# Kernel optimization log

Measured on AMD Instinct MI355X. Metric: run time of the kernel, lower is better.

## Reference

```python
import jax, jax.numpy as jnp
import numpy as np

B, S, S2 = 4, 4096, 2048
D, SCAF_D, H = 1024, 768, 8
HD = D // H
BLEND = 0.5
SIG_HALF = 0.6224593312018546  # sigmoid(0.5), initial sparsity_factor
K = max(1, min(S, int(S * SIG_HALF)))  # 2549, static top-k size


def setup_inputs() -> dict:
    key = jax.random.key(0)
    ks = jax.random.split(key, 12)
    s = 0.02
    return {
        "base_hidden": jax.random.normal(ks[0], (B, S, D), jnp.float32),
        "scaffold_hidden": jax.random.normal(ks[1], (B, S2, SCAF_D), jnp.float32),
        "scaffold_proj_w": jax.random.normal(ks[2], (D, SCAF_D), jnp.float32) * s,
        "scaffold_proj_b": jnp.zeros((D,), jnp.float32),
        "topk_w": jax.random.normal(ks[3], (1, D), jnp.float32) * s,
        "topk_b": jnp.zeros((1,), jnp.float32),
        "in_proj_w": jax.random.normal(ks[4], (3 * D, D), jnp.float32) * s,
        "in_proj_b": jnp.zeros((3 * D,), jnp.float32),
        "out_proj_w": jax.random.normal(ks[5], (D, D), jnp.float32) * s,
        "out_proj_b": jnp.zeros((D,), jnp.float32),
        "gate_w": jax.random.normal(ks[6], (1, D), jnp.float32) * s,
        "gate_b": jnp.zeros((1,), jnp.float32),
        "confidence_threshold": jnp.array([0.65], jnp.float32),
    }


def reference(base_hidden, scaffold_hidden, scaffold_proj_w, scaffold_proj_b,
              topk_w, topk_b, in_proj_w, in_proj_b, out_proj_w, out_proj_b,
              gate_w, gate_b, confidence_threshold):
    # scaffold projection: [B,S2,SCAF_D] -> [B,S2,D]
    scaf = jnp.einsum('bsk,dk->bsd', scaffold_hidden, scaffold_proj_w) + scaffold_proj_b
    conf = jnp.mean(jnp.linalg.norm(scaf, axis=-1))

    # learned top-k token selection on base tokens
    scores = jnp.einsum('bsd,od->bso', base_hidden, topk_w)[..., 0] + topk_b[0]  # [B,S]
    _, idx = jax.lax.top_k(scores, K)  # [B,K]
    sparse = jnp.take_along_axis(base_hidden, idx[:, :, None], axis=1)  # [B,K,D]

    # multihead cross-attention: query=sparse tokens, key/value=scaffold
    wq, wk, wv = in_proj_w[:D], in_proj_w[D:2 * D], in_proj_w[2 * D:]
    bq, bk, bv = in_proj_b[:D], in_proj_b[D:2 * D], in_proj_b[2 * D:]
    q = (jnp.einsum('bkd,ed->bke', sparse, wq) + bq).reshape(B, K, H, HD)
    k = (jnp.einsum('bsd,ed->bse', scaf, wk) + bk).reshape(B, S2, H, HD)
    v = (jnp.einsum('bsd,ed->bse', scaf, wv) + bv).reshape(B, S2, H, HD)
    att = jnp.einsum('bqhd,bkhd->bhqk', q, k) / jnp.sqrt(jnp.float32(HD))
    p = jax.nn.softmax(att, axis=-1)
    o = jnp.einsum('bhqk,bkhd->bqhd', p, v).reshape(B, K, D)
    attn_out = jnp.einsum('bkd,ed->bke', o, out_proj_w) + out_proj_b  # [B,K,D]

    # scatter attended tokens back into the full sequence
    b_idx = jnp.arange(B)[:, None]
    attn_full = base_hidden.at[b_idx, idx].set(attn_out)  # [B,S,D]

    gate = jax.nn.sigmoid(jnp.einsum('bsd,od->bso', base_hidden, gate_w) + gate_b)  # [B,S,1]
    augmented = base_hidden + gate * attn_full
    fused = (1.0 - BLEND) * base_hidden + BLEND * augmented
    return jnp.where(conf > confidence_threshold[0], fused, base_hidden)
```

## Files before the change

kernel.cpp:

```cpp
#include <hip/hip_runtime.h>
#include <hip/hip_bf16.h>

typedef unsigned short u16;
typedef unsigned int   u32;
typedef __bf16 bf16x8 __attribute__((ext_vector_type(8)));
typedef float  f32x4  __attribute__((ext_vector_type(4)));

#define B_     4
#define S_     4096
#define S2_    2048
#define D_     1024
#define SCAFD_ 768
#define H_     8
#define HD_    128
#define KSEL_  2549
#define MROWS_ (B_ * KSEL_)
#define QK_SCALE 0.08838834764831845f
#define QBLKS_ ((KSEL_ + 127) / 128)
#define ANWG_  (QBLKS_ * H_ * B_)

#define CN0_ (D_ * SCAFD_ / 4)
#define CN1_ (3 * D_ * D_ / 4)
#define CN2_ (D_ * D_ / 4)

__device__ __forceinline__ float b2f(u16 u){
  union { u32 i; float f; } c; c.i = ((u32)u) << 16; return c.f;
}
__device__ __forceinline__ u16 f2b(float f){
  u32 x = __float_as_uint(f);
  u32 r = x + 0x7fffu + ((x >> 16) & 1u);
  return (u16)(r >> 16);
}
__device__ __forceinline__ u32 pk2(float lo, float hi){
  return (u32)f2b(lo) | ((u32)f2b(hi) << 16);
}
__device__ __forceinline__ f32x4 mfma16(bf16x8 a, bf16x8 b, f32x4 c){
  return __builtin_amdgcn_mfma_f32_16x16x32_bf16(a, b, c, 0, 0, 0);
}
__device__ __forceinline__ void gl_lds16(const u16* g, u16* l){
  __builtin_amdgcn_global_load_lds((const __attribute__((address_space(1))) void*)g,
                                   (__attribute__((address_space(3))) void*)l, 16, 0, 0);
}

__global__ void CrossAttentionFuser_65798898975031_kernel() {}

__global__ __launch_bounds__(256) void cast3_k(
    const float* __restrict__ s0, u16* __restrict__ d0,
    const float* __restrict__ s1, u16* __restrict__ d1,
    const float* __restrict__ s2, u16* __restrict__ d2)
{
  int i = blockIdx.x * 256 + threadIdx.x;
  const float* s; u16* d; int j = i;
  if (j < CN0_){ s = s0; d = d0; }
  else if (j < CN0_ + CN1_){ j -= CN0_; s = s1; d = d1; }
  else { j -= CN0_ + CN1_; s = s2; d = d2; }
  float4 v = ((const float4*)s)[j];
  uint2 o; o.x = pk2(v.x, v.y); o.y = pk2(v.z, v.w);
  ((uint2*)d)[j] = o;
}

__global__ __launch_bounds__(256) void scores_gate_k(
    const float* __restrict__ base, const float* __restrict__ tw, const float* __restrict__ tb,
    const float* __restrict__ gw, const float* __restrict__ gb,
    float* __restrict__ scores, float* __restrict__ gate, float* __restrict__ conf_sum)
{
  int t = threadIdx.x, wave = t >> 6, lane = t & 63;
  if (blockIdx.x == 0 && t == 0) conf_sum[0] = 0.f;
  int row = blockIdx.x * 4 + wave;
  const float* bp  = base + (size_t)row * D_ + lane * 16;
  const float* twp = tw + lane * 16;
  const float* gwp = gw + lane * 16;
  float sd = 0.f, gd = 0.f;
  #pragma unroll
  for (int c = 0; c < 4; c++){
    float4 b4 = *(const float4*)(bp  + c * 4);
    float4 t4 = *(const float4*)(twp + c * 4);
    float4 g4 = *(const float4*)(gwp + c * 4);
    sd = fmaf(b4.x, t4.x, sd); sd = fmaf(b4.y, t4.y, sd);
    sd = fmaf(b4.z, t4.z, sd); sd = fmaf(b4.w, t4.w, sd);
    gd = fmaf(b4.x, g4.x, gd); gd = fmaf(b4.y, g4.y, gd);
    gd = fmaf(b4.z, g4.z, gd); gd = fmaf(b4.w, g4.w, gd);
  }
  #pragma unroll
  for (int off = 32; off > 0; off >>= 1){
    sd += __shfl_xor(sd, off);
    gd += __shfl_xor(gd, off);
  }
  if (lane == 0){
    scores[row] = sd + tb[0];
    gate[row]   = 1.f / (1.f + __expf(-(gd + gb[0])));
  }
}

__global__ __launch_bounds__(1024) void topk_sel_k(
    const float* __restrict__ scores, int* __restrict__ sel_rows, int* __restrict__ sel_pos)
{
  __shared__ unsigned long long keys[4096];
  __shared__ int hist[256];
  __shared__ int wsum[16], woff[16];
  __shared__ int sh_found, sh_Kr;
  int b = blockIdx.x, t = threadIdx.x;
  for (int i = t; i < 4096; i += 1024){
    float s = scores[b * 4096 + i];
    u32 bits = __float_as_uint(s);
    bits = (bits & 0x80000000u) ? ~bits : (bits | 0x80000000u);
    keys[i] = ((unsigned long long)bits << 12) | (unsigned long long)(4095 - i);
  }
  __syncthreads();
  int Kr = KSEL_;
  unsigned long long prefix = 0;
  int shift_prev = 44;
  const int shifts[6] = {36, 28, 20, 12, 4, 0};
  for (int lev = 0; lev < 6; lev++){
    int shift = shifts[lev];
    if (t < 256) hist[t] = 0;
    __syncthreads();
    for (int i = t; i < 4096; i += 1024){
      unsigned long long k = keys[i];
      if ((k >> shift_prev) == prefix)
        atomicAdd(&hist[(int)((k >> shift) & 255)], 1);
    }
    __syncthreads();
    if (t == 0){
      int cum = 0, fb = 0;
      for (int bk = 255; bk >= 0; bk--){
        int h = hist[bk];
        if (cum + h >= Kr){ fb = bk; break; }
        cum += h;
      }
      sh_found = fb; sh_Kr = Kr - cum;
    }
    __syncthreads();
    int gap = shift_prev - shift;
    prefix = (prefix << gap) | (unsigned long long)(sh_found & ((1 << gap) - 1));
    Kr = sh_Kr;
    shift_prev = shift;
    __syncthreads();
  }
  unsigned long long T = prefix;
  int base_i = t * 4;
  int cnt = 0, flags = 0;
  #pragma unroll
  for (int j = 0; j < 4; j++){
    if (keys[base_i + j] >= T){ cnt++; flags |= 1 << j; }
  }
  int lane = t & 63, wv = t >> 6;
  int sc = cnt;
  #pragma unroll
  for (int off = 1; off < 64; off <<= 1){
    int v = __shfl_up(sc, off);
    if (lane >= off) sc += v;
  }
  if (lane == 63) wsum[wv] = sc;
  __syncthreads();
  if (t < 16){
    int acc = 0;
    for (int j = 0; j < 16; j++){ if (j < t) acc += wsum[j]; }
    woff[t] = acc;
  }
  __syncthreads();
  int pos = sc - cnt + woff[wv];
  #pragma unroll
  for (int j = 0; j < 4; j++){
    int s = base_i + j;
    int p = -1;
    if ((flags >> j) & 1){
      p = pos++;
      sel_rows[b * KSEL_ + p] = b * S_ + s;
    }
    sel_pos[b * S_ + s] = p;
  }
}

__global__ __launch_bounds__(256) void gemm128(
    const void* __restrict__ Aptr, int aMode,
    const u16* __restrict__ Wb, const float* __restrict__ bias,
    void* __restrict__ Cptr, int outMode, float outScale,
    const int* __restrict__ rowidx, int M, int N, int Kd)
{
  __shared__ __align__(16) u16 At[128 * 32];
  __shared__ __align__(16) u16 Wt[128 * 32];
  int m0 = blockIdx.x * 128, n0 = blockIdx.y * 128;
  int t = threadIdx.x;
  int lane = t & 63, quad = lane >> 4, l15 = lane & 15;
  int wave = t >> 6, wm = wave >> 1, wn = wave & 1;
  int srow = t >> 2, chunk = t & 3;
  const float* apf[2];
  const u16*   apb[2];
  const u16*   wpp[2];
  #pragma unroll
  for (int r = 0; r < 2; r++){
    int rr = m0 + r * 64 + srow; if (rr > M - 1) rr = M - 1;
    int gr = rowidx ? rowidx[rr] : rr;
    apf[r] = (const float*)Aptr + (size_t)gr * Kd + chunk * 8;
    apb[r] = (const u16*)Aptr   + (size_t)gr * Kd + chunk * 8;
    wpp[r] = Wb + (size_t)(n0 + r * 64 + srow) * Kd + chunk * 8;
  }
  f32x4 acc[4][4];
  #pragma unroll
  for (int mi = 0; mi < 4; mi++){
    #pragma unroll
    for (int ni = 0; ni < 4; ni++){
      f32x4 z = {0.f, 0.f, 0.f, 0.f};
      acc[mi][ni] = z;
    }
  }
  for (int k0 = 0; k0 < Kd; k0 += 32){
    __syncthreads();
    #pragma unroll
    for (int r = 0; r < 2; r++){
      gl_lds16(wpp[r] + k0, Wt + r * 2048 + t * 8);
    }
    if (aMode == 0){
      #pragma unroll
      for (int r = 0; r < 2; r++){
        gl_lds16(apb[r] + k0, At + r * 2048 + t * 8);
      }
    } else {
      #pragma unroll
      for (int r = 0; r < 2; r++){
        float4 a0 = *(const float4*)(apf[r] + k0);
        float4 a1 = *(const float4*)(apf[r] + k0 + 4);
        uint4 av;
        av.x = pk2(a0.x, a0.y); av.y = pk2(a0.z, a0.w);
        av.z = pk2(a1.x, a1.y); av.w = pk2(a1.z, a1.w);
        *(uint4*)(At + r * 2048 + t * 8) = av;
      }
    }
    __syncthreads();
    bf16x8 afr[4], bfr[4];
    #pragma unroll
    for (int mi = 0; mi < 4; mi++){
      afr[mi] = *(const bf16x8*)(At + (wm * 64 + mi * 16 + l15) * 32 + quad * 8);
    }
    #pragma unroll
    for (int ni = 0; ni < 4; ni++){
      bfr[ni] = *(const bf16x8*)(Wt + (wn * 64 + ni * 16 + l15) * 32 + quad * 8);
    }
    #pragma unroll
    for (int mi = 0; mi < 4; mi++){
      #pragma unroll
      for (int ni = 0; ni < 4; ni++){
        acc[mi][ni] = mfma16(afr[mi], bfr[ni], acc[mi][ni]);
      }
    }
  }
  #pragma unroll
  for (int ni = 0; ni < 4; ni++){
    int col = n0 + wn * 64 + ni * 16 + l15;
    float bs = bias[col];
    #pragma unroll
    for (int mi = 0; mi < 4; mi++){
      #pragma unroll
      for (int r = 0; r < 4; r++){
        int row = m0 + wm * 64 + mi * 16 + quad * 4 + r;
        if (row < M){
          float val = (acc[mi][ni][r] + bs) * outScale;
          if (outMode == 0){
            ((u16*)Cptr)[(size_t)row * N + col] = f2b(val);
          } else if (outMode == 1){
            int bb = row >> 11, s2 = row & 2047;
            int hh = col >> 7,  hd = col & 127;
            ((u16*)Cptr)[((size_t)((bb * 8 + hh) * 128 + hd) << 11) + s2] = f2b(val);
          } else {
            ((float*)Cptr)[(size_t)row * N + col] = val;
          }
        }
      }
    }
  }
}

__global__ __launch_bounds__(256) void conf_k(const u16* __restrict__ scaf, float* __restrict__ conf_sum){
  int t = threadIdx.x, wave = t >> 6, lane = t & 63;
  float acc = 0.f;
  for (int i = 0; i < 32; i++){
    int row = blockIdx.x * 128 + wave * 32 + i;
    const u16* rp = scaf + (size_t)row * D_ + lane * 16;
    uint4 v0 = *(const uint4*)rp, v1 = *(const uint4*)(rp + 8);
    float ss = 0.f;
    u32 w[8];
    w[0]=v0.x; w[1]=v0.y; w[2]=v0.z; w[3]=v0.w;
    w[4]=v1.x; w[5]=v1.y; w[6]=v1.z; w[7]=v1.w;
    #pragma unroll
    for (int j = 0; j < 8; j++){
      float lo = b2f(w[j] & 0xffff), hi = b2f(w[j] >> 16);
      ss = fmaf(lo, lo, ss);
      ss = fmaf(hi, hi, ss);
    }
    #pragma unroll
    for (int off = 32; off > 0; off >>= 1){
      ss += __shfl_xor(ss, off);
    }
    if (lane == 0) acc += sqrtf(ss);
  }
  if (lane == 0) atomicAdd(conf_sum, acc);
}

__global__ __launch_bounds__(256, 3) void attn_k(
    const u16* __restrict__ Q, const u16* __restrict__ Kb,
    const u16* __restrict__ Vt, u16* __restrict__ O, int KS)
{
  __shared__ __align__(16) u16 Klds[64 * 128];
  __shared__ __align__(16) u16 Vtlds[128 * 64];
  int o = blockIdx.x;
  int id = (o & 7) * (ANWG_ >> 3) + (o >> 3);
  int qblk = id % QBLKS_;
  int rest = id / QBLKS_;
  int h = rest & 7, b = rest >> 3;
  int t = threadIdx.x, wave = t >> 6, lane = t & 63, quad = lane >> 4, l15 = lane & 15;
  int qbase = qblk * 128 + wave * 32;
  int e7 = l15 & 7;

  bf16x8 aq[2][4];
  #pragma unroll
  for (int ti = 0; ti < 2; ti++){
    int qr = qbase + ti * 16 + l15; if (qr > KS - 1) qr = KS - 1;
    const u16* qp = Q + (size_t)(b * KS + qr) * D_ + h * HD_;
    #pragma unroll
    for (int c = 0; c < 4; c++){
      aq[ti][c] = *(const bf16x8*)(qp + c * 32 + quad * 8);
    }
  }
  float l_i[2];
  f32x4 oa[2][8];
  #pragma unroll
  for (int ti = 0; ti < 2; ti++){
    l_i[ti] = 0.f;
    #pragma unroll
    for (int n = 0; n < 8; n++){
      f32x4 z = {0.f, 0.f, 0.f, 0.f};
      oa[ti][n] = z;
    }
  }
  int krow = t >> 2, kc4 = t & 3;
  int vhd  = t >> 1, vhalf = t & 1;
  int krow7 = krow & 7, vhd7 = vhd & 7;
  const u16* kgp = Kb + (size_t)(b * S2_ + krow) * D_ + h * HD_ + kc4 * 8;
  const u16* vgp = Vt + (size_t)((b * H_ + h) * HD_ + vhd) * S2_ + vhalf * 32;
  int srcA = 32 * (quad & 1) + l15;
  int srcB = srcA + 16;
  bool hiq = (lane & 32) != 0;

  for (int s0 = 0; s0 < S2_; s0 += 64){
    __syncthreads();
    #pragma unroll
    for (int i = 0; i < 4; i++){
      int kch = (kc4 + 4 * i) ^ krow7;
      int vch = (vhalf * 4 + i) ^ vhd7;
      *(uint4*)&Klds[krow * 128 + kch * 8]  = *(const uint4*)(kgp + 32 * i);
      *(uint4*)&Vtlds[vhd * 64 + vch * 8]   = *(const uint4*)(vgp + 8 * i);
    }
    kgp += (size_t)64 * D_;
    vgp += 64;
    __syncthreads();

    f32x4 sc[2][4];
    #pragma unroll
    for (int tt = 0; tt < 4; tt++){
      f32x4 z = {0.f, 0.f, 0.f, 0.f};
      sc[0][tt] = z; sc[1][tt] = z;
    }
    #pragma unroll
    for (int c = 0; c < 4; c++){
      bf16x8 q0 = aq[0][c], q1 = aq[1][c];
      int kch = (c * 4 + quad) ^ e7;
      #pragma unroll
      for (int tt = 0; tt < 4; tt++){
        bf16x8 kf = *(const bf16x8*)&Klds[(tt * 16 + l15) * 128 + kch * 8];
        sc[0][tt] = mfma16(kf, q0, sc[0][tt]);
        sc[1][tt] = mfma16(kf, q1, sc[1][tt]);
      }
    }

    u32 pp[2][4][2];
    #pragma unroll
    for (int ti = 0; ti < 2; ti++){
      float ps = 0.f;
      #pragma unroll
      for (int tt = 0; tt < 4; tt++){
        float e0 = __expf(sc[ti][tt][0]);
        float e1 = __expf(sc[ti][tt][1]);
        float e2 = __expf(sc[ti][tt][2]);
        float e3 = __expf(sc[ti][tt][3]);
        ps += (e0 + e1) + (e2 + e3);
        pp[ti][tt][0] = pk2(e0, e1);
        pp[ti][tt][1] = pk2(e2, e3);
      }
      ps += __shfl_xor(ps, 16);
      ps += __shfl_xor(ps, 32);
      l_i[ti] += ps;
    }

    #pragma unroll
    for (int g = 0; g < 2; g++){
      union { u32 w[4]; bf16x8 v; } pf0, pf1;
      {
        u32 a0 = (u32)__shfl((int)pp[0][2*g][0],   srcA);
        u32 b0 = (u32)__shfl((int)pp[0][2*g+1][0], srcA);
        u32 a1 = (u32)__shfl((int)pp[0][2*g][1],   srcA);
        u32 b1 = (u32)__shfl((int)pp[0][2*g+1][1], srcA);
        u32 a2 = (u32)__shfl((int)pp[0][2*g][0],   srcB);
        u32 b2 = (u32)__shfl((int)pp[0][2*g+1][0], srcB);
        u32 a3 = (u32)__shfl((int)pp[0][2*g][1],   srcB);
        u32 b3 = (u32)__shfl((int)pp[0][2*g+1][1], srcB);
        pf0.w[0] = hiq ? b0 : a0;
        pf0.w[1] = hiq ? b1 : a1;
        pf0.w[2] = hiq ? b2 : a2;
        pf0.w[3] = hiq ? b3 : a3;
      }
      {
        u32 a0 = (u32)__shfl((int)pp[1][2*g][0],   srcA);
        u32 b0 = (u32)__shfl((int)pp[1][2*g+1][0], srcA);
        u32 a1 = (u32)__shfl((int)pp[1][2*g][1],   srcA);
        u32 b1 = (u32)__shfl((int)pp[1][2*g+1][1], srcA);
        u32 a2 = (u32)__shfl((int)pp[1][2*g][0],   srcB);
        u32 b2 = (u32)__shfl((int)pp[1][2*g+1][0], srcB);
        u32 a3 = (u32)__shfl((int)pp[1][2*g][1],   srcB);
        u32 b3 = (u32)__shfl((int)pp[1][2*g+1][1], srcB);
        pf1.w[0] = hiq ? b0 : a0;
        pf1.w[1] = hiq ? b1 : a1;
        pf1.w[2] = hiq ? b2 : a2;
        pf1.w[3] = hiq ? b3 : a3;
      }
      int vch = (g * 4 + quad) ^ e7;
      #pragma unroll
      for (int n = 0; n < 8; n++){
        bf16x8 vf = *(const bf16x8*)&Vtlds[(n * 16 + l15) * 64 + vch * 8];
        oa[0][n] = mfma16(vf, pf0.v, oa[0][n]);
        oa[1][n] = mfma16(vf, pf1.v, oa[1][n]);
      }
    }
  }
  #pragma unroll
  for (int ti = 0; ti < 2; ti++){
    int qrow = qbase + ti * 16 + l15;
    if (qrow < KS){
      float inv = 1.f / l_i[ti];
      size_t rowoff = (size_t)(b * KS + qrow) * D_ + h * HD_;
      #pragma unroll
      for (int n = 0; n < 8; n++){
        uint2 wv;
        wv.x = pk2(oa[ti][n][0] * inv, oa[ti][n][1] * inv);
        wv.y = pk2(oa[ti][n][2] * inv, oa[ti][n][3] * inv);
        *(uint2*)&O[rowoff + n * 16 + quad * 4] = wv;
      }
    }
  }
}

__global__ __launch_bounds__(256) void final_fuse_k(
    const float* __restrict__ base, const float* __restrict__ gate, const int* __restrict__ sel_pos,
    const float* __restrict__ attnout, const float* __restrict__ conf_sum,
    const float* __restrict__ thr, float* __restrict__ out)
{
  int row = blockIdx.x;
  int d0 = threadIdx.x * 4;
  size_t off = (size_t)row * D_ + d0;
  float4 bv = *(const float4*)(base + off);
  bool conf = (conf_sum[0] * (1.0f / (B_ * S2_))) > thr[0];
  float4 ov;
  if (!conf){
    ov = bv;
  } else {
    float g = gate[row] * 0.5f;
    int p = sel_pos[row];
    if (p >= 0){
      int bb = row >> 12;
      float4 av = *(const float4*)(attnout + (size_t)(bb * KSEL_ + p) * D_ + d0);
      ov.x = fmaf(g, av.x, bv.x);
      ov.y = fmaf(g, av.y, bv.y);
      ov.z = fmaf(g, av.z, bv.z);
      ov.w = fmaf(g, av.w, bv.w);
    } else {
      ov.x = fmaf(g, bv.x, bv.x);
      ov.y = fmaf(g, bv.y, bv.y);
      ov.z = fmaf(g, bv.z, bv.z);
      ov.w = fmaf(g, bv.w, bv.w);
    }
  }
  *(float4*)(out + off) = ov;
}

extern "C" void kernel_launch(void* const* d_in, const int* in_sizes, int n_in,
                              void* d_out, int out_size, void* d_ws, size_t ws_size,
                              hipStream_t stream)
{
  (void)in_sizes; (void)n_in; (void)out_size; (void)ws_size;
  const float* base  = (const float*)d_in[0];
  const float* scafh = (const float*)d_in[1];
  const float* spw   = (const float*)d_in[2];
  const float* spb   = (const float*)d_in[3];
  const float* tw    = (const float*)d_in[4];
  const float* tb    = (const float*)d_in[5];
  const float* ipw   = (const float*)d_in[6];
  const float* ipb   = (const float*)d_in[7];
  const float* opw   = (const float*)d_in[8];
  const float* opb   = (const float*)d_in[9];
  const float* gw    = (const float*)d_in[10];
  const float* gb    = (const float*)d_in[11];
  const float* thr   = (const float*)d_in[12];
  float* out = (float*)d_out;

  char* ws = (char*)d_ws;
  size_t off = 0;
  auto alloc = [&](size_t bytes) -> void* {
    void* p = ws + off; off += (bytes + 255) & ~(size_t)255; return p;
  };
  float* conf_sum = (float*)alloc(4);
  float* scores   = (float*)alloc((size_t)B_ * S_ * 4);
  float* gate     = (float*)alloc((size_t)B_ * S_ * 4);
  int*   sel_rows = (int*)alloc((size_t)MROWS_ * 4);
  int*   sel_pos  = (int*)alloc((size_t)B_ * S_ * 4);
  u16*   spwb     = (u16*)alloc((size_t)D_ * SCAFD_ * 2);
  u16*   ipwb     = (u16*)alloc((size_t)3 * D_ * D_ * 2);
  u16*   opwb     = (u16*)alloc((size_t)D_ * D_ * 2);
  u16*   scaf     = (u16*)alloc((size_t)B_ * S2_ * D_ * 2);
  u16*   kbuf     = (u16*)alloc((size_t)B_ * S2_ * D_ * 2);
  u16*   vt       = (u16*)alloc((size_t)B_ * S2_ * D_ * 2);
  u16*   qbuf     = (u16*)alloc((size_t)MROWS_ * D_ * 2);
  float* attnout  = (float*)scaf;

  cast3_k<<<dim3((CN0_ + CN1_ + CN2_) / 256), 256, 0, stream>>>(
      spw, spwb, ipw, ipwb, opw, opwb);

  scores_gate_k<<<dim3(B_ * S_ / 4), 256, 0, stream>>>(base, tw, tb, gw, gb, scores, gate, conf_sum);
  topk_sel_k<<<dim3(B_), 1024, 0, stream>>>(scores, sel_rows, sel_pos);
  gemm128<<<dim3(B_ * S2_ / 128, D_ / 128), 256, 0, stream>>>(
      scafh, 1, spwb, spb, scaf, 0, 1.f, nullptr, B_ * S2_, D_, SCAFD_);
  conf_k<<<dim3(B_ * S2_ / 128), 256, 0, stream>>>(scaf, conf_sum);
  gemm128<<<dim3(B_ * S2_ / 128, D_ / 128), 256, 0, stream>>>(
      scaf, 0, ipwb + (size_t)D_ * D_, ipb + D_, kbuf, 0, 1.f, nullptr, B_ * S2_, D_, D_);
  gemm128<<<dim3(B_ * S2_ / 128, D_ / 128), 256, 0, stream>>>(
      scaf, 0, ipwb + (size_t)2 * D_ * D_, ipb + 2 * D_, vt, 1, 1.f, nullptr, B_ * S2_, D_, D_);
  gemm128<<<dim3((MROWS_ + 127) / 128, D_ / 128), 256, 0, stream>>>(
      base, 1, ipwb, ipb, qbuf, 0, QK_SCALE, sel_rows, MROWS_, D_, D_);
  attn_k<<<dim3(ANWG_), 256, 0, stream>>>(qbuf, kbuf, vt, qbuf, KSEL_);
  gemm128<<<dim3((MROWS_ + 127) / 128, D_ / 128), 256, 0, stream>>>(
      qbuf, 0, opwb, opb, attnout, 2, 1.f, nullptr, MROWS_, D_, D_);
  final_fuse_k<<<dim3(B_ * S_), 256, 0, stream>>>(
      base, gate, sel_pos, attnout, conf_sum, thr, out);
}
```

Before: 586.9 us.

## Fuse K/V projection GEMMs and shrink attention workgroups to 64 queries

The separate K and V projection GEMMs become one GEMM with N=2*D. A new output mode writes the first half as row-major K and the second half transposed into the V layout, which saves a launch and a second pass over the scaffold activations. The attention kernel now uses 128 threads (2 waves, 64 queries per workgroup) instead of 256. This doubles the number of workgroups for better CU fill, but each workgroup has to reload the K/V tiles, so K/V traffic to LDS per query doubles.

```diff
diff --git a/kernel.cpp b/kernel.cpp
--- a/kernel.cpp
+++ b/kernel.cpp
@@ -16,7 +16,7 @@
 #define KSEL_  2549
 #define MROWS_ (B_ * KSEL_)
 #define QK_SCALE 0.08838834764831845f
-#define QBLKS_ ((KSEL_ + 127) / 128)
+#define QBLKS_ ((KSEL_ + 63) / 64)
 #define ANWG_  (QBLKS_ * H_ * B_)
 
 #define CN0_ (D_ * SCAFD_ / 4)
@@ -262,8 +262,18 @@
             int bb = row >> 11, s2 = row & 2047;
             int hh = col >> 7,  hd = col & 127;
             ((u16*)Cptr)[((size_t)((bb * 8 + hh) * 128 + hd) << 11) + s2] = f2b(val);
+          } else if (outMode == 2){
+            ((float*)Cptr)[(size_t)row * N + col] = val;
           } else {
-            ((float*)Cptr)[(size_t)row * N + col] = val;
+            if (col < D_){
+              ((u16*)Cptr)[(size_t)row * D_ + col] = f2b(val);
+            } else {
+              int bb = row >> 11, s2 = row & 2047;
+              int cc = col - D_;
+              int hh = cc >> 7, hd = cc & 127;
+              u16* vtp = (u16*)Cptr + (size_t)B_ * S2_ * D_;
+              vtp[((size_t)((bb * 8 + hh) * 128 + hd) << 11) + s2] = f2b(val);
+            }
           }
         }
       }
@@ -297,7 +307,7 @@
   if (lane == 0) atomicAdd(conf_sum, acc);
 }
 
-__global__ __launch_bounds__(256, 3) void attn_k(
+__global__ __launch_bounds__(128) void attn_k(
     const u16* __restrict__ Q, const u16* __restrict__ Kb,
     const u16* __restrict__ Vt, u16* __restrict__ O, int KS)
 {
@@ -309,7 +319,7 @@
   int rest = id / QBLKS_;
   int h = rest & 7, b = rest >> 3;
   int t = threadIdx.x, wave = t >> 6, lane = t & 63, quad = lane >> 4, l15 = lane & 15;
-  int qbase = qblk * 128 + wave * 32;
+  int qbase = qblk * 64 + wave * 32;
   int e7 = l15 & 7;
 
   bf16x8 aq[2][4];
@@ -333,11 +343,11 @@
       oa[ti][n] = z;
     }
   }
-  int krow = t >> 2, kc4 = t & 3;
-  int vhd  = t >> 1, vhalf = t & 1;
+  int krow = t >> 1, kc2 = t & 1;
+  int vhd  = t;
   int krow7 = krow & 7, vhd7 = vhd & 7;
-  const u16* kgp = Kb + (size_t)(b * S2_ + krow) * D_ + h * HD_ + kc4 * 8;
-  const u16* vgp = Vt + (size_t)((b * H_ + h) * HD_ + vhd) * S2_ + vhalf * 32;
+  const u16* kgp = Kb + (size_t)(b * S2_ + krow) * D_ + h * HD_ + kc2 * 64;
+  const u16* vgp = Vt + (size_t)((b * H_ + h) * HD_ + vhd) * S2_;
   int srcA = 32 * (quad & 1) + l15;
   int srcB = srcA + 16;
   bool hiq = (lane & 32) != 0;
@@ -345,11 +355,11 @@
   for (int s0 = 0; s0 < S2_; s0 += 64){
     __syncthreads();
     #pragma unroll
-    for (int i = 0; i < 4; i++){
-      int kch = (kc4 + 4 * i) ^ krow7;
-      int vch = (vhalf * 4 + i) ^ vhd7;
-      *(uint4*)&Klds[krow * 128 + kch * 8]  = *(const uint4*)(kgp + 32 * i);
-      *(uint4*)&Vtlds[vhd * 64 + vch * 8]   = *(const uint4*)(vgp + 8 * i);
+    for (int i = 0; i < 8; i++){
+      int kch = (kc2 * 8 + i) ^ krow7;
+      int vch = i ^ vhd7;
+      *(uint4*)&Klds[krow * 128 + kch * 8] = *(const uint4*)(kgp + 8 * i);
+      *(uint4*)&Vtlds[vhd * 64 + vch * 8]  = *(const uint4*)(vgp + 8 * i);
     }
     kgp += (size_t)64 * D_;
     vgp += 64;
@@ -516,8 +526,9 @@
   u16*   ipwb     = (u16*)alloc((size_t)3 * D_ * D_ * 2);
   u16*   opwb     = (u16*)alloc((size_t)D_ * D_ * 2);
   u16*   scaf     = (u16*)alloc((size_t)B_ * S2_ * D_ * 2);
-  u16*   kbuf     = (u16*)alloc((size_t)B_ * S2_ * D_ * 2);
-  u16*   vt       = (u16*)alloc((size_t)B_ * S2_ * D_ * 2);
+  u16*   kvbuf    = (u16*)alloc((size_t)2 * B_ * S2_ * D_ * 2);
+  u16*   kbuf     = kvbuf;
+  u16*   vt       = kvbuf + (size_t)B_ * S2_ * D_;
   u16*   qbuf     = (u16*)alloc((size_t)MROWS_ * D_ * 2);
   float* attnout  = (float*)scaf;
 
@@ -529,13 +540,11 @@
   gemm128<<<dim3(B_ * S2_ / 128, D_ / 128), 256, 0, stream>>>(
       scafh, 1, spwb, spb, scaf, 0, 1.f, nullptr, B_ * S2_, D_, SCAFD_);
   conf_k<<<dim3(B_ * S2_ / 128), 256, 0, stream>>>(scaf, conf_sum);
-  gemm128<<<dim3(B_ * S2_ / 128, D_ / 128), 256, 0, stream>>>(
-      scaf, 0, ipwb + (size_t)D_ * D_, ipb + D_, kbuf, 0, 1.f, nullptr, B_ * S2_, D_, D_);
-  gemm128<<<dim3(B_ * S2_ / 128, D_ / 128), 256, 0, stream>>>(
-      scaf, 0, ipwb + (size_t)2 * D_ * D_, ipb + 2 * D_, vt, 1, 1.f, nullptr, B_ * S2_, D_, D_);
+  gemm128<<<dim3(B_ * S2_ / 128, 2 * D_ / 128), 256, 0, stream>>>(
+      scaf, 0, ipwb + (size_t)D_ * D_, ipb + D_, kvbuf, 3, 1.f, nullptr, B_ * S2_, 2 * D_, D_);
   gemm128<<<dim3((MROWS_ + 127) / 128, D_ / 128), 256, 0, stream>>>(
       base, 1, ipwb, ipb, qbuf, 0, QK_SCALE, sel_rows, MROWS_, D_, D_);
-  attn_k<<<dim3(ANWG_), 256, 0, stream>>>(qbuf, kbuf, vt, qbuf, KSEL_);
+  attn_k<<<dim3(ANWG_), 128, 0, stream>>>(qbuf, kbuf, vt, qbuf, KSEL_);
   gemm128<<<dim3((MROWS_ + 127) / 128, D_ / 128), 256, 0, stream>>>(
       qbuf, 0, opwb, opb, attnout, 2, 1.f, nullptr, MROWS_, D_, D_);
   final_fuse_k<<<dim3(B_ * S_), 256, 0, stream>>>(
```

After: 849.3 us. +44.7%, slower.

## Fuse K and V projections into one GEMM and prefetch K/V tiles in attention

Applied to the files above, without the earlier changes.

The K and V projection GEMMs become a single launch over N=2048 with a new output mode. That mode writes K row-major and V transposed into one contiguous buffer, which raises the workgroup count and avoids a second read pass over scaf. The attention kernel now loads the next K/V tile from global memory into registers while the current tile is in use, so load latency can overlap with the MFMA work. This adds register pressure from the eight uint4 prefetch registers, which may lower occupancy.

```diff
diff --git a/kernel.cpp b/kernel.cpp
--- a/kernel.cpp
+++ b/kernel.cpp
@@ -262,8 +262,18 @@
             int bb = row >> 11, s2 = row & 2047;
             int hh = col >> 7,  hd = col & 127;
             ((u16*)Cptr)[((size_t)((bb * 8 + hh) * 128 + hd) << 11) + s2] = f2b(val);
+          } else if (outMode == 2){
+            ((float*)Cptr)[(size_t)row * N + col] = val;
           } else {
-            ((float*)Cptr)[(size_t)row * N + col] = val;
+            if (col < D_){
+              ((u16*)Cptr)[(size_t)row * D_ + col] = f2b(val);
+            } else {
+              int bb = row >> 11, s2 = row & 2047;
+              int cc = col - D_;
+              int hh = cc >> 7, hd = cc & 127;
+              u16* vtp = (u16*)Cptr + (size_t)B_ * S2_ * D_;
+              vtp[((size_t)((bb * 8 + hh) * 128 + hd) << 11) + s2] = f2b(val);
+            }
           }
         }
       }
@@ -342,17 +352,33 @@
   int srcB = srcA + 16;
   bool hiq = (lane & 32) != 0;
 
+  uint4 kreg[4], vreg[4];
+  #pragma unroll
+  for (int i = 0; i < 4; i++){
+    kreg[i] = *(const uint4*)(kgp + 32 * i);
+    vreg[i] = *(const uint4*)(vgp + 8 * i);
+  }
+  kgp += (size_t)64 * D_;
+  vgp += 64;
+
   for (int s0 = 0; s0 < S2_; s0 += 64){
     __syncthreads();
     #pragma unroll
     for (int i = 0; i < 4; i++){
       int kch = (kc4 + 4 * i) ^ krow7;
       int vch = (vhalf * 4 + i) ^ vhd7;
-      *(uint4*)&Klds[krow * 128 + kch * 8]  = *(const uint4*)(kgp + 32 * i);
-      *(uint4*)&Vtlds[vhd * 64 + vch * 8]   = *(const uint4*)(vgp + 8 * i);
-    }
-    kgp += (size_t)64 * D_;
-    vgp += 64;
+      *(uint4*)&Klds[krow * 128 + kch * 8] = kreg[i];
+      *(uint4*)&Vtlds[vhd * 64 + vch * 8]  = vreg[i];
+    }
+    if (s0 + 64 < S2_){
+      #pragma unroll
+      for (int i = 0; i < 4; i++){
+        kreg[i] = *(const uint4*)(kgp + 32 * i);
+        vreg[i] = *(const uint4*)(vgp + 8 * i);
+      }
+      kgp += (size_t)64 * D_;
+      vgp += 64;
+    }
     __syncthreads();
 
     f32x4 sc[2][4];
@@ -516,8 +542,9 @@
   u16*   ipwb     = (u16*)alloc((size_t)3 * D_ * D_ * 2);
   u16*   opwb     = (u16*)alloc((size_t)D_ * D_ * 2);
   u16*   scaf     = (u16*)alloc((size_t)B_ * S2_ * D_ * 2);
-  u16*   kbuf     = (u16*)alloc((size_t)B_ * S2_ * D_ * 2);
-  u16*   vt       = (u16*)alloc((size_t)B_ * S2_ * D_ * 2);
+  u16*   kvbuf    = (u16*)alloc((size_t)2 * B_ * S2_ * D_ * 2);
+  u16*   kbuf     = kvbuf;
+  u16*   vt       = kvbuf + (size_t)B_ * S2_ * D_;
   u16*   qbuf     = (u16*)alloc((size_t)MROWS_ * D_ * 2);
   float* attnout  = (float*)scaf;
 
@@ -529,10 +556,8 @@
   gemm128<<<dim3(B_ * S2_ / 128, D_ / 128), 256, 0, stream>>>(
       scafh, 1, spwb, spb, scaf, 0, 1.f, nullptr, B_ * S2_, D_, SCAFD_);
   conf_k<<<dim3(B_ * S2_ / 128), 256, 0, stream>>>(scaf, conf_sum);
-  gemm128<<<dim3(B_ * S2_ / 128, D_ / 128), 256, 0, stream>>>(
-      scaf, 0, ipwb + (size_t)D_ * D_, ipb + D_, kbuf, 0, 1.f, nullptr, B_ * S2_, D_, D_);
-  gemm128<<<dim3(B_ * S2_ / 128, D_ / 128), 256, 0, stream>>>(
-      scaf, 0, ipwb + (size_t)2 * D_ * D_, ipb + 2 * D_, vt, 1, 1.f, nullptr, B_ * S2_, D_, D_);
+  gemm128<<<dim3(B_ * S2_ / 128, 2 * D_ / 128), 256, 0, stream>>>(
+      scaf, 0, ipwb + (size_t)D_ * D_, ipb + D_, kvbuf, 3, 1.f, nullptr, B_ * S2_, 2 * D_, D_);
   gemm128<<<dim3((MROWS_ + 127) / 128, D_ / 128), 256, 0, stream>>>(
       base, 1, ipwb, ipb, qbuf, 0, QK_SCALE, sel_rows, MROWS_, D_, D_);
   attn_k<<<dim3(ANWG_), 256, 0, stream>>>(qbuf, kbuf, vt, qbuf, KSEL_);
```

Measured after the change: 725.5 us. 1.24x slower.
